# Kernel tuning notes

Measured on AMD Instinct MI355X. Metric: run time of the kernel, lower is better.

## Reference

```python
import jax, jax.numpy as jnp
import numpy as np

N_NODES = 100000


def _spmm(edge_index, edge_weight, x):
    # out[i] = sum_j A[i, j] * x[j]; row=dst=edge_index[0], col=src=edge_index[1]
    dst, src = edge_index[0], edge_index[1]
    msgs = edge_weight[:, None] * x[src]  # [E, d]
    return jax.ops.segment_sum(msgs, dst, num_segments=N_NODES)


def setup_inputs() -> dict:
    key = jax.random.key(0)
    k1, k2, k3, k4 = jax.random.split(key, 4)
    N, E, D = N_NODES, 3200000, 64
    features = jax.random.normal(k1, (N, D), dtype=jnp.float32)
    edge_weight = jax.random.uniform(k2, (E,), dtype=jnp.float32)
    dst = jax.random.randint(k3, (E,), 0, N)
    src = jax.random.randint(k4, (E,), 0, N)
    edge_index = jnp.stack([dst, src]).astype(jnp.int64)
    return {"features": features, "edge_weight": edge_weight,
            "edge_index": edge_index, "degree": 2}


def reference(features, edge_weight, edge_index, degree):
    # SGC: features = adj @ features, repeated `degree` times (no learned params)
    x = features
    for _ in range(degree):
        x = _spmm(edge_index, edge_weight, x)
    return x
```

## Files before the change

### kernel.cpp

```cpp
#include <hip/hip_runtime.h>
#include <hip/hip_fp16.h>

#define N_NODES 100000
#define DFEAT 64
#define CH 8192
#define NBK 391
#define NPB 256
#define CAPB 9216

__device__ __forceinline__ int block_scan_excl_512(int v, int* sb, int tid, int* total)
{
    const int lane = tid & 63, wid = tid >> 6;
    int inc = v;
#pragma unroll
    for (int o = 1; o < 64; o <<= 1) {
        int t = __shfl_up(inc, o, 64);
        if (lane >= o) inc += t;
    }
    if (lane == 63) sb[wid] = inc;
    __syncthreads();
    if (wid == 0) {
        int wv = (lane < 8) ? sb[lane] : 0;
        int winc = wv;
#pragma unroll
        for (int o = 1; o < 8; o <<= 1) {
            int t = __shfl_up(winc, o, 64);
            if (lane >= o) winc += t;
        }
        if (lane < 8) sb[8 + lane] = winc - wv;
    }
    __syncthreads();
    *total = sb[15] + sb[7];
    return sb[8 + wid] + inc - v;
}

__global__ __launch_bounds__(512) void sort_chunks(
    const int* __restrict__ dst, const int* __restrict__ src,
    const float* __restrict__ w,
    unsigned* __restrict__ recs_g, unsigned char* __restrict__ dloc_g,
    int* __restrict__ off_T, int E, int nch)
{
    __shared__ int  hist[NBK + 1];
    __shared__ int  cursor[NBK];
    __shared__ int  sb[16];
    __shared__ unsigned      lrec[CH];
    __shared__ unsigned char ldl[CH];

    const int chunk = blockIdx.x;
    const int base  = chunk * CH;
    const int n     = min(CH, E - base);
    const int tid   = threadIdx.x;

    if (tid < NBK + 1) hist[tid] = 0;
    __syncthreads();

    for (int k = tid; k < n; k += 512) atomicAdd(&hist[dst[base + k] >> 8], 1);
    __syncthreads();

    int v = (tid < NBK) ? hist[tid] : 0;
    int tot;
    int excl = block_scan_excl_512(v, sb, tid, &tot);
    if (tid <= NBK) {
        off_T[(size_t)tid * nch + chunk] = base + excl;
        if (tid < NBK) cursor[tid] = excl;
    }
    __syncthreads();

    for (int k = tid; k < n; k += 512) {
        int d = dst[base + k];
        int pos = atomicAdd(&cursor[d >> 8], 1);
        unsigned wq = (unsigned)__float2int_rn(w[base + k] * 32768.0f);
        if (wq > 32767u) wq = 32767u;
        lrec[pos] = (unsigned)src[base + k] | (wq << 17);
        ldl[pos]  = (unsigned char)(d & 255);
    }
    __syncthreads();

    int4* rg = (int4*)(recs_g + base);
    const int4* rl = (const int4*)lrec;
    for (int k = tid; k < ((n + 3) >> 2); k += 512) rg[k] = rl[k];
    int4* dg = (int4*)(dloc_g + base);
    const int4* dl4 = (const int4*)ldl;
    for (int k = tid; k < ((n + 15) >> 4); k += 512) dg[k] = dl4[k];
}

__global__ __launch_bounds__(64) void bucket_tot(
    const int* __restrict__ off_T, int* __restrict__ gtot, int nch)
{
    const int b = blockIdx.x;
    const int lane = threadIdx.x;
    const int* r0 = off_T + (size_t)b * nch;
    const int* r1 = off_T + (size_t)(b + 1) * nch;
    int s = 0;
    for (int c = lane; c < nch; c += 64) s += r1[c] - r0[c];
    for (int o = 32; o > 0; o >>= 1) s += __shfl_down(s, o, 64);
    if (lane == 0) gtot[b] = s;
}

__global__ __launch_bounds__(512) void bucket_scan(
    const int* __restrict__ gtot, int* __restrict__ gbase)
{
    __shared__ int sb[16];
    const int tid = threadIdx.x;
    int v = (tid < NBK) ? gtot[tid] : 0;
    int tot;
    int excl = block_scan_excl_512(v, sb, tid, &tot);
    if (tid < NBK) gbase[tid] = excl;
}

__global__ __launch_bounds__(512) void build_csr(
    const int* __restrict__ off_T, const unsigned* __restrict__ recs_g,
    const unsigned char* __restrict__ dloc_g, const int* __restrict__ gbase,
    unsigned* __restrict__ edges_s, int* __restrict__ row_ptr, int nch, int E)
{
    __shared__ unsigned      lrecL[CAPB];
    __shared__ unsigned char dlocL[CAPB];
    __shared__ int gsrcL[512];
    __shared__ int lenL[512];
    __shared__ int ldstL[512];
    __shared__ int histL[NPB];
    __shared__ int cursorL[NPB];
    __shared__ int sb[16];

    const int b   = blockIdx.x;
    const int tid = threadIdx.x;
    const int gb  = gbase[b];

    int len = 0;
    if (tid < nch) {
        int a0 = off_T[(size_t)b * nch + tid];
        int a1 = off_T[(size_t)(b + 1) * nch + tid];
        gsrcL[tid] = a0;
        len = a1 - a0;
        lenL[tid] = len;
    }
    int cnt;
    int dstoff = block_scan_excl_512((tid < nch) ? len : 0, sb, tid, &cnt);
    if (tid < nch) ldstL[tid] = dstoff;
    if (tid < NPB) histL[tid] = 0;
    __syncthreads();

    const int grp = tid >> 4;
    const int gl  = tid & 15;
    for (int c = grp; c < nch; c += 32) {
        int s = gsrcL[c], d = ldstL[c], L = lenL[c];
        for (int k = gl; k < L; k += 16) {
            lrecL[d + k] = recs_g[s + k];
            dlocL[d + k] = dloc_g[s + k];
        }
    }
    __syncthreads();

    for (int k = tid; k < cnt; k += 512) atomicAdd(&histL[dlocL[k]], 1);
    __syncthreads();

    int hv = (tid < NPB) ? histL[tid] : 0;
    int htot;
    int hexcl = block_scan_excl_512(hv, sb, tid, &htot);
    if (tid < NPB) {
        int i = b * NPB + tid;
        if (i < N_NODES) row_ptr[i] = gb + hexcl;
        cursorL[tid] = gb + hexcl;
    }
    if (b == NBK - 1 && tid == 0) row_ptr[N_NODES] = E;
    __syncthreads();

    for (int k = tid; k < cnt; k += 512) {
        int pos = atomicAdd(&cursorL[dlocL[k]], 1);
        edges_s[pos] = lrecL[k];
    }
}

__global__ __launch_bounds__(256) void cast_f2h(
    const float* __restrict__ in, __half* __restrict__ out, int n2)
{
    int i = blockIdx.x * blockDim.x + threadIdx.x;
    if (i < n2) {
        float2 f = ((const float2*)in)[i];
        ((__half2*)out)[i] = __floats2half2_rn(f.x, f.y);
    }
}

template <int OUT_FP16>
__global__ __launch_bounds__(256) void spmm_csr(
    const int* __restrict__ row_ptr,
    const unsigned* __restrict__ edges,
    const uint2* __restrict__ x4,
    void* __restrict__ outv)
{
    int node = __builtin_amdgcn_readfirstlane(blockIdx.x * 4 + (int)(threadIdx.x >> 6));
    if (node >= N_NODES) return;
    const int lane = threadIdx.x & 63;
    const int g    = lane >> 4;
    const int gl   = lane & 15;

    const int beg = row_ptr[node];
    const int end = row_ptr[node + 1];

    float a0 = 0.f, a1 = 0.f, a2 = 0.f, a3 = 0.f;
    int e0 = beg;
    const int nblk = (end - beg) >> 4;

#define ACC4(v, w) do {                                            \
        __half2 _h0 = *(__half2*)&(v).x;                           \
        __half2 _h1 = *(__half2*)&(v).y;                           \
        a0 += (w) * __low2float(_h0);  a1 += (w) * __high2float(_h0); \
        a2 += (w) * __low2float(_h1);  a3 += (w) * __high2float(_h1); \
    } while (0)

    if (nblk > 0) {
        unsigned n0 = edges[e0 +  0 + g];
        unsigned n1 = edges[e0 +  4 + g];
        unsigned n2 = edges[e0 +  8 + g];
        unsigned n3 = edges[e0 + 12 + g];
        e0 += 16;

        for (int b = 0; b < nblk; ++b) {
            uint2 v0 = x4[(size_t)(n0 & 0x1FFFF) * 16 + gl];
            uint2 v1 = x4[(size_t)(n1 & 0x1FFFF) * 16 + gl];
            uint2 v2 = x4[(size_t)(n2 & 0x1FFFF) * 16 + gl];
            uint2 v3 = x4[(size_t)(n3 & 0x1FFFF) * 16 + gl];

            float w0 = (float)(n0 >> 17), w1 = (float)(n1 >> 17);
            float w2 = (float)(n2 >> 17), w3 = (float)(n3 >> 17);

            if (b + 1 < nblk) {
                n0 = edges[e0 +  0 + g];
                n1 = edges[e0 +  4 + g];
                n2 = edges[e0 +  8 + g];
                n3 = edges[e0 + 12 + g];
                e0 += 16;
            }

            ACC4(v0, w0);
            ACC4(v1, w1);
            ACC4(v2, w2);
            ACC4(v3, w3);
        }
    }

    for (; e0 + 4 <= end; e0 += 4) {
        unsigned r = edges[e0 + g];
        uint2 v = x4[(size_t)(r & 0x1FFFF) * 16 + gl];
        float w = (float)(r >> 17);
        ACC4(v, w);
    }
    {
        int rem = end - e0;
        if (g < rem) {
            unsigned r = edges[e0 + g];
            uint2 v = x4[(size_t)(r & 0x1FFFF) * 16 + gl];
            float w = (float)(r >> 17);
            ACC4(v, w);
        }
    }
#undef ACC4

    a0 += __shfl_xor(a0, 16, 64);  a0 += __shfl_xor(a0, 32, 64);
    a1 += __shfl_xor(a1, 16, 64);  a1 += __shfl_xor(a1, 32, 64);
    a2 += __shfl_xor(a2, 16, 64);  a2 += __shfl_xor(a2, 32, 64);
    a3 += __shfl_xor(a3, 16, 64);  a3 += __shfl_xor(a3, 32, 64);

    if (g == 0) {
        const float k = 1.0f / 32768.0f;
        float s0 = a0 * k, s1 = a1 * k, s2 = a2 * k, s3 = a3 * k;
        if (OUT_FP16) {
            __half2 p0 = __floats2half2_rn(s0, s1);
            __half2 p1 = __floats2half2_rn(s2, s3);
            uint2 pv;
            pv.x = *(unsigned*)&p0;
            pv.y = *(unsigned*)&p1;
            ((uint2*)outv)[(size_t)node * 16 + gl] = pv;
        } else {
            ((float4*)outv)[(size_t)node * 16 + gl] = make_float4(s0, s1, s2, s3);
        }
    }
}

extern "C" void kernel_launch(void* const* d_in, const int* in_sizes, int n_in,
                              void* d_out, int out_size, void* d_ws, size_t ws_size,
                              hipStream_t stream) {
    const float* features = (const float*)d_in[0];
    const float* edge_w   = (const float*)d_in[1];
    const int*   edge_idx = (const int*)d_in[2];

    const int E = in_sizes[1];
    const int* dst = edge_idx;
    const int* src = edge_idx + E;

    const int nch = (E + CH - 1) / CH;

    char* ws = (char*)d_ws;
    unsigned*      recs_g  = (unsigned*)ws;      ws += (size_t)nch * CH * sizeof(unsigned);
    unsigned char* dloc_g  = (unsigned char*)ws; ws += (size_t)nch * CH;
    unsigned*      edges_s = (unsigned*)ws;      ws += (size_t)E * sizeof(unsigned);
    __half*        tmp_h   = (__half*)ws;        ws += (size_t)N_NODES * DFEAT * sizeof(__half);
    int*           off_T   = (int*)ws;           ws += (size_t)(NBK + 1) * nch * sizeof(int);
    int*           row_ptr = (int*)ws;           ws += (size_t)(N_NODES + 1) * sizeof(int);
    int*           gtot    = (int*)ws;           ws += (size_t)NBK * sizeof(int);
    int*           gbase   = (int*)ws;           ws += (size_t)NBK * sizeof(int);

    __half* features_h = (__half*)recs_g;

    float* out = (float*)d_out;

    sort_chunks<<<nch, 512, 0, stream>>>(dst, src, edge_w, recs_g, dloc_g, off_T, E, nch);
    bucket_tot <<<NBK, 64, 0, stream>>>(off_T, gtot, nch);
    bucket_scan<<<1, 512, 0, stream>>>(gtot, gbase);
    build_csr  <<<NBK, 512, 0, stream>>>(off_T, recs_g, dloc_g, gbase, edges_s, row_ptr, nch, E);

    const int n2 = N_NODES * DFEAT / 2;
    cast_f2h<<<(n2 + 255) / 256, 256, 0, stream>>>(features, features_h, n2);

    const int ngrid = (N_NODES + 3) / 4;
    spmm_csr<1><<<ngrid, 256, 0, stream>>>(row_ptr, edges_s, (const uint2*)features_h, tmp_h);
    spmm_csr<0><<<ngrid, 256, 0, stream>>>(row_ptr, edges_s, (const uint2*)tmp_h, out);
}
```

Baseline: 270.0 us.

## Fold bucket offset scan into build_csr and fuse fp16 cast into sort

Removes the bucket_tot and bucket_scan kernels. Each build_csr block now derives its global base by summing its row of chunk offsets and subtracting a host-computed constant, which assumes the offset layout places each chunk's start at chunk*CH. The feature fp16 cast moves into sort_chunks as a grid-stride tail, so cast_f2h is gone. Workspace aliasing changes so the fp16 features get their own buffer and the intermediate reuses recs_g. Together this cuts three kernel launches and their serialization.

```diff
diff --git a/kernel.cpp b/kernel.cpp
--- a/kernel.cpp
+++ b/kernel.cpp
@@ -38,7 +38,8 @@
     const int* __restrict__ dst, const int* __restrict__ src,
     const float* __restrict__ w,
     unsigned* __restrict__ recs_g, unsigned char* __restrict__ dloc_g,
-    int* __restrict__ off_T, int E, int nch)
+    int* __restrict__ off_T, int E, int nch,
+    const float* __restrict__ feat_in, __half* __restrict__ feat_out, int n2)
 {
     __shared__ int  hist[NBK + 1];
     __shared__ int  cursor[NBK];
@@ -82,36 +83,19 @@
     int4* dg = (int4*)(dloc_g + base);
     const int4* dl4 = (const int4*)ldl;
     for (int k = tid; k < ((n + 15) >> 4); k += 512) dg[k] = dl4[k];
-}
-
-__global__ __launch_bounds__(64) void bucket_tot(
-    const int* __restrict__ off_T, int* __restrict__ gtot, int nch)
-{
-    const int b = blockIdx.x;
-    const int lane = threadIdx.x;
-    const int* r0 = off_T + (size_t)b * nch;
-    const int* r1 = off_T + (size_t)(b + 1) * nch;
-    int s = 0;
-    for (int c = lane; c < nch; c += 64) s += r1[c] - r0[c];
-    for (int o = 32; o > 0; o >>= 1) s += __shfl_down(s, o, 64);
-    if (lane == 0) gtot[b] = s;
-}
-
-__global__ __launch_bounds__(512) void bucket_scan(
-    const int* __restrict__ gtot, int* __restrict__ gbase)
-{
-    __shared__ int sb[16];
-    const int tid = threadIdx.x;
-    int v = (tid < NBK) ? gtot[tid] : 0;
-    int tot;
-    int excl = block_scan_excl_512(v, sb, tid, &tot);
-    if (tid < NBK) gbase[tid] = excl;
+
+    const int gstride = gridDim.x * 512;
+    for (int i = blockIdx.x * 512 + tid; i < n2; i += gstride) {
+        float2 f = ((const float2*)feat_in)[i];
+        ((__half2*)feat_out)[i] = __floats2half2_rn(f.x, f.y);
+    }
 }
 
 __global__ __launch_bounds__(512) void build_csr(
     const int* __restrict__ off_T, const unsigned* __restrict__ recs_g,
-    const unsigned char* __restrict__ dloc_g, const int* __restrict__ gbase,
-    unsigned* __restrict__ edges_s, int* __restrict__ row_ptr, int nch, int E)
+    const unsigned char* __restrict__ dloc_g,
+    unsigned* __restrict__ edges_s, int* __restrict__ row_ptr,
+    int nch, int E, int scan_const)
 {
     __shared__ unsigned      lrecL[CAPB];
     __shared__ unsigned char dlocL[CAPB];
@@ -124,18 +108,22 @@
 
     const int b   = blockIdx.x;
     const int tid = threadIdx.x;
-    const int gb  = gbase[b];
-
-    int len = 0;
+
+    int len = 0, a0v = 0;
     if (tid < nch) {
         int a0 = off_T[(size_t)b * nch + tid];
         int a1 = off_T[(size_t)(b + 1) * nch + tid];
         gsrcL[tid] = a0;
+        a0v = a0;
         len = a1 - a0;
         lenL[tid] = len;
     }
+    int rowsum;
+    block_scan_excl_512(a0v, sb, tid, &rowsum);
+    const int gb = rowsum - scan_const;
+
     int cnt;
-    int dstoff = block_scan_excl_512((tid < nch) ? len : 0, sb, tid, &cnt);
+    int dstoff = block_scan_excl_512(len, sb, tid, &cnt);
     if (tid < nch) ldstL[tid] = dstoff;
     if (tid < NPB) histL[tid] = 0;
     __syncthreads();
@@ -168,16 +156,6 @@
     for (int k = tid; k < cnt; k += 512) {
         int pos = atomicAdd(&cursorL[dlocL[k]], 1);
         edges_s[pos] = lrecL[k];
-    }
-}
-
-__global__ __launch_bounds__(256) void cast_f2h(
-    const float* __restrict__ in, __half* __restrict__ out, int n2)
-{
-    int i = blockIdx.x * blockDim.x + threadIdx.x;
-    if (i < n2) {
-        float2 f = ((const float2*)in)[i];
-        ((__half2*)out)[i] = __floats2half2_rn(f.x, f.y);
     }
 }
 
@@ -294,25 +272,24 @@
     unsigned*      recs_g  = (unsigned*)ws;      ws += (size_t)nch * CH * sizeof(unsigned);
     unsigned char* dloc_g  = (unsigned char*)ws; ws += (size_t)nch * CH;
     unsigned*      edges_s = (unsigned*)ws;      ws += (size_t)E * sizeof(unsigned);
-    __half*        tmp_h   = (__half*)ws;        ws += (size_t)N_NODES * DFEAT * sizeof(__half);
+    __half*        feat_h  = (__half*)ws;        ws += (size_t)N_NODES * DFEAT * sizeof(__half);
     int*           off_T   = (int*)ws;           ws += (size_t)(NBK + 1) * nch * sizeof(int);
     int*           row_ptr = (int*)ws;           ws += (size_t)(N_NODES + 1) * sizeof(int);
-    int*           gtot    = (int*)ws;           ws += (size_t)NBK * sizeof(int);
-    int*           gbase   = (int*)ws;           ws += (size_t)NBK * sizeof(int);
-
-    __half* features_h = (__half*)recs_g;
+
+    __half* tmp_h = (__half*)recs_g;
 
     float* out = (float*)d_out;
 
-    sort_chunks<<<nch, 512, 0, stream>>>(dst, src, edge_w, recs_g, dloc_g, off_T, E, nch);
-    bucket_tot <<<NBK, 64, 0, stream>>>(off_T, gtot, nch);
-    bucket_scan<<<1, 512, 0, stream>>>(gtot, gbase);
-    build_csr  <<<NBK, 512, 0, stream>>>(off_T, recs_g, dloc_g, gbase, edges_s, row_ptr, nch, E);
+    const int scan_const = (int)((long long)CH * (((long long)(nch - 1) * nch) / 2));
 
     const int n2 = N_NODES * DFEAT / 2;
-    cast_f2h<<<(n2 + 255) / 256, 256, 0, stream>>>(features, features_h, n2);
+
+    sort_chunks<<<nch, 512, 0, stream>>>(dst, src, edge_w, recs_g, dloc_g, off_T,
+                                         E, nch, features, feat_h, n2);
+    build_csr  <<<NBK, 512, 0, stream>>>(off_T, recs_g, dloc_g, edges_s, row_ptr,
+                                         nch, E, scan_const);
 
     const int ngrid = (N_NODES + 3) / 4;
-    spmm_csr<1><<<ngrid, 256, 0, stream>>>(row_ptr, edges_s, (const uint2*)features_h, tmp_h);
+    spmm_csr<1><<<ngrid, 256, 0, stream>>>(row_ptr, edges_s, (const uint2*)feat_h, tmp_h);
     spmm_csr<0><<<ngrid, 256, 0, stream>>>(row_ptr, edges_s, (const uint2*)tmp_h, out);
 }
```

Measured after the change: 270.3 us. Within noise of the previous version (+0.1%).
